# Kernel tuning notes

Measured on AMD Instinct MI355X. Metric: run time of the kernel, lower is better.

## Reference

```python
import jax, jax.numpy as jnp
import numpy as np

B, N, D, FF = 4096, 8, 256, 2048
EPS = 1e-5


def _layernorm(x, gamma, beta):
    mu = jnp.mean(x, axis=-1, keepdims=True)
    var = jnp.mean((x - mu) ** 2, axis=-1, keepdims=True)
    return (x - mu) * jax.lax.rsqrt(var + EPS) * gamma + beta


def _tt_product(x, w):
    # x: [b, d_in, n], w: [d_in, d_out, n]
    # h[:, :, k] = sum_i x[:, :, i] @ w[:, :, (k - i) % n]  (circular contraction)
    n = x.shape[-1]
    k = jnp.arange(n)
    idx = (k[:, None] - k[None, :]) % n          # [k, i]
    wg = w[:, :, idx]                            # [d_in, d_out, k, i]
    return jnp.einsum('bdi,doki->bok', x, wg)    # [b, d_out, n]


def setup_inputs() -> dict:
    key = jax.random.key(0)
    ks = jax.random.split(key, 12)
    xav = lambda k, shp, fi, fo: jax.random.uniform(k, shp, jnp.float32, -1.0, 1.0) * np.sqrt(6.0 / (fi + fo))
    return {
        'ent_seq': jax.random.normal(ks[0], (B, N, D), jnp.float32),
        'w_in': xav(ks[1], (D, D, N), D, D),
        'w_out': xav(ks[2], (D, D, N), D, D),
        'W1': xav(ks[3], (FF, D), D, FF),
        'bias1': jnp.zeros((FF,), jnp.float32),
        'W2': xav(ks[4], (D, FF), FF, D),
        'bias2': jnp.zeros((D,), jnp.float32),
        'gamma1': jnp.ones((D,), jnp.float32),
        'beta1': jnp.zeros((D,), jnp.float32),
        'gamma2': jnp.ones((D,), jnp.float32),
        'beta2': jnp.zeros((D,), jnp.float32),
    }


def reference(ent_seq, w_in, w_out, W1, bias1, W2, bias2, gamma1, beta1, gamma2, beta2):
    # self-attention-like block (dropout = identity in eval mode)
    xn = _layernorm(ent_seq, gamma1, beta1)          # [B, N, D]
    xp = jnp.transpose(xn, (0, 2, 1))                # [B, D, N]
    half = xp.shape[0] // 2
    h = jnp.concatenate([_tt_product(xp[:half], w_in),
                         _tt_product(xp[half:], w_out)], axis=0)
    x = ent_seq + jnp.transpose(h, (0, 2, 1))        # residual
    # FFN block
    yn = _layernorm(x, gamma2, beta2)
    ff = jax.nn.relu(yn @ W1.T + bias1) @ W2.T + bias2
    return x + ff
```

## Files before the change

### kernel.cpp

```cpp
#include <hip/hip_runtime.h>
#include <hip/hip_bf16.h>

typedef unsigned short ushort_t;
typedef __attribute__((ext_vector_type(8))) short bf16x8;
typedef __attribute__((ext_vector_type(4))) float f32x4;

#define B_SZ 4096
#define N_SZ 8
#define D_SZ 256
#define FF_SZ 2048
#define M_SZ (B_SZ * N_SZ)
#define WELEM (D_SZ * D_SZ * N_SZ)

__device__ inline float b2f(ushort_t u) {
    union { unsigned int i; float f; } t; t.i = ((unsigned int)u) << 16; return t.f;
}
__device__ inline ushort_t f2b(float f) {
    union { unsigned int i; float f; } t; t.f = f;
    unsigned int i = t.i;
    unsigned int r = (i + 0x7fffu + ((i >> 16) & 1u)) >> 16;
    return (ushort_t)r;
}

__device__ inline void gl2lds16(const ushort_t* g, ushort_t* l) {
    __builtin_amdgcn_global_load_lds((const __attribute__((address_space(1))) void*)g,
                                     (__attribute__((address_space(3))) void*)l, 16, 0, 0);
}

__global__ __launch_bounds__(256) void convert_weights(const float* __restrict__ w_in,
                                                       const float* __restrict__ w_out,
                                                       const float* __restrict__ W1,
                                                       const float* __restrict__ W2,
                                                       ushort_t* __restrict__ bt_in,
                                                       ushort_t* __restrict__ bt_out,
                                                       ushort_t* __restrict__ W1b,
                                                       ushort_t* __restrict__ W2b) {
    __shared__ float tile[64][65];
    const int bid = blockIdx.x;
    const int t = threadIdx.x;
    if (bid < 256) {
        const float* w = (bid < 128) ? w_in : w_out;
        ushort_t* bt = (bid < 128) ? bt_in : bt_out;
        const int id = bid & 127;
        const int d10 = (id >> 5) * 64;
        const int j0  = (id & 31) * 64;
#pragma unroll
        for (int it = 0; it < 16; ++it) {
            const int d1l = it * 4 + (t >> 6);
            const int jl = t & 63;
            tile[d1l][jl] = w[(size_t)(d10 + d1l) * 2048 + j0 + jl];
        }
        __syncthreads();
#pragma unroll
        for (int it = 0; it < 16; ++it) {
            const int jl = it * 4 + (t >> 6);
            const int d1l = t & 63;
            const int j = j0 + jl;
            bt[(size_t)(j >> 3) * 2048 + (j & 7) * 256 + d10 + d1l] = f2b(tile[d1l][jl]);
        }
    } else {
        const int id = bid - 256;
        const float* w = (id < 256) ? W1 : W2;
        ushort_t* o = (id < 256) ? W1b : W2b;
        const size_t base = (size_t)(id & 255) * 2048 + t * 8;
        const float4 a = *(const float4*)&w[base];
        const float4 b = *(const float4*)&w[base + 4];
        *(ushort4*)&o[base]     = make_ushort4(f2b(a.x), f2b(a.y), f2b(a.z), f2b(a.w));
        *(ushort4*)&o[base + 4] = make_ushort4(f2b(b.x), f2b(b.y), f2b(b.z), f2b(b.w));
    }
}

__global__ __launch_bounds__(256) void ln_fast(const float* __restrict__ xin,
                                               const float* __restrict__ gam,
                                               const float* __restrict__ bet,
                                               ushort_t* __restrict__ out) {
    const int wave = threadIdx.x >> 6;
    const int lane = threadIdx.x & 63;
    const size_t row = (size_t)blockIdx.x * 4 + wave;
    const float4 v = *(const float4*)&xin[row * 256 + lane * 4];
    float s = v.x + v.y + v.z + v.w;
    float q = v.x * v.x + v.y * v.y + v.z * v.z + v.w * v.w;
#pragma unroll
    for (int off = 1; off < 64; off <<= 1) {
        s += __shfl_xor(s, off, 64);
        q += __shfl_xor(q, off, 64);
    }
    const float mu = s * (1.0f / 256.0f);
    const float var = q * (1.0f / 256.0f) - mu * mu;
    const float rs = rsqrtf(var + 1e-5f);
    const float4 g = *(const float4*)&gam[lane * 4];
    const float4 b = *(const float4*)&bet[lane * 4];
    ushort4 o;
    o.x = f2b((v.x - mu) * rs * g.x + b.x);
    o.y = f2b((v.y - mu) * rs * g.y + b.y);
    o.z = f2b((v.z - mu) * rs * g.z + b.z);
    o.w = f2b((v.w - mu) * rs * g.w + b.w);
    *(ushort4*)&out[row * 256 + lane * 4] = o;
}

__global__ __launch_bounds__(256, 2) void tt_ln2(const ushort_t* __restrict__ A,
                                                 const ushort_t* __restrict__ Bt0,
                                                 const ushort_t* __restrict__ Bt1,
                                                 const float* __restrict__ g2,
                                                 const float* __restrict__ be2,
                                                 const float* __restrict__ entf,
                                                 ushort_t* __restrict__ yn,
                                                 ushort_t* __restrict__ xb) {
    __shared__ __attribute__((aligned(16))) ushort_t As[64 * 64];
    __shared__ __attribute__((aligned(16))) ushort_t Bs[256 * 64];
    __shared__ float red_s[64 * 4];
    __shared__ float red_q[64 * 4];

    const int t = threadIdx.x;
    const int lb = ((blockIdx.x & 1) << 8) | (blockIdx.x >> 1);
    const int m0 = lb * 64;
    const int lane = t & 63;
    const int wc = t >> 6;
    const int l16 = lane & 15, quad = lane >> 4;
    const int tr = t >> 3;
    const int csw = (((t & 7) ^ (tr & 7)) << 3);

    const ushort_t* Bt = (m0 >= M_SZ / 2) ? Bt1 : Bt0;

    f32x4 acc[4][4];
#pragma unroll
    for (int i = 0; i < 4; i++)
#pragma unroll
        for (int j = 0; j < 4; j++) acc[i][j] = (f32x4)(0.0f);

#pragma unroll 1
    for (int kt = 0; kt < 32; ++kt) {
        const int kg = kt * 64;
        __syncthreads();
#pragma unroll
        for (int p = 0; p < 2; ++p) {
            const int mrow = m0 + p * 32 + tr;
            const int kcol = kg + csw;
            const int s = kcol >> 8;
            const ushort_t* gA = A + (size_t)((mrow & ~7) + (((mrow & 7) - s) & 7)) * 256 + (kcol & 255);
            gl2lds16(gA, As + p * 2048 + t * 8);
        }
#pragma unroll
        for (int p = 0; p < 8; ++p) {
            gl2lds16(Bt + (size_t)(p * 32 + tr) * 2048 + kg + csw, Bs + p * 2048 + t * 8);
        }
        __syncthreads();

#pragma unroll
        for (int kk = 0; kk < 2; ++kk) {
            const int ac = ((((kk << 2) | quad) ^ (l16 & 7)) << 3);
            bf16x8 af[4], bfv[4];
#pragma unroll
            for (int i = 0; i < 4; i++) af[i]  = *(const bf16x8*)&As[(i * 16 + l16) * 64 + ac];
#pragma unroll
            for (int j = 0; j < 4; j++) bfv[j] = *(const bf16x8*)&Bs[(wc * 64 + j * 16 + l16) * 64 + ac];
#pragma unroll
            for (int i = 0; i < 4; i++)
#pragma unroll
                for (int j = 0; j < 4; j++)
                    acc[i][j] = __builtin_amdgcn_mfma_f32_16x16x32_bf16(af[i], bfv[j], acc[i][j], 0, 0, 0);
        }
    }

    int c[4];
#pragma unroll
    for (int j = 0; j < 4; j++) c[j] = wc * 64 + j * 16 + l16;
#pragma unroll
    for (int i = 0; i < 4; i++) {
#pragma unroll
        for (int r = 0; r < 4; r++) {
            const int rl = i * 16 + quad * 4 + r;
            const size_t grow = (size_t)(m0 + rl) * 256;
            float s = 0.0f, q = 0.0f;
#pragma unroll
            for (int j = 0; j < 4; j++) {
                float v = acc[i][j][r] + entf[grow + c[j]];
                acc[i][j][r] = v;
                s += v;
                q += v * v;
            }
#pragma unroll
            for (int off = 1; off < 16; off <<= 1) {
                s += __shfl_xor(s, off, 64);
                q += __shfl_xor(q, off, 64);
            }
            if (l16 == 0) { red_s[rl * 4 + wc] = s; red_q[rl * 4 + wc] = q; }
        }
    }
    __syncthreads();
#pragma unroll
    for (int i = 0; i < 4; i++) {
#pragma unroll
        for (int r = 0; r < 4; r++) {
            const int rl = i * 16 + quad * 4 + r;
            const size_t grow = (size_t)(m0 + rl) * 256;
            const float4 ss = *(const float4*)&red_s[rl * 4];
            const float4 qq = *(const float4*)&red_q[rl * 4];
            const float S = ss.x + ss.y + ss.z + ss.w;
            const float Q = qq.x + qq.y + qq.z + qq.w;
            const float mu = S * (1.0f / 256.0f);
            const float var = Q * (1.0f / 256.0f) - mu * mu;
            const float rs = rsqrtf(var + 1e-5f);
#pragma unroll
            for (int j = 0; j < 4; j++) {
                const float v = acc[i][j][r];
                yn[grow + c[j]] = f2b((v - mu) * rs * g2[c[j]] + be2[c[j]]);
                xb[grow + c[j]] = f2b(v);
            }
        }
    }
}

__global__ __launch_bounds__(256, 2) void ff_fused(const ushort_t* __restrict__ yn,
                                                   const ushort_t* __restrict__ W1b,
                                                   const ushort_t* __restrict__ W2b,
                                                   const float* __restrict__ bias1,
                                                   const float* __restrict__ bias2,
                                                   const ushort_t* __restrict__ xb,
                                                   float* __restrict__ out) {
    __shared__ __attribute__((aligned(16))) ushort_t As[64 * 64];
    __shared__ __attribute__((aligned(16))) ushort_t Bs[256 * 64];
    __shared__ __attribute__((aligned(16))) ushort_t Hc[64 * 256];

    const int t = threadIdx.x;
    const int m0 = blockIdx.x * 64;
    const int lane = t & 63;
    const int wc = t >> 6;
    const int l16 = lane & 15, quad = lane >> 4;
    const int tr = t >> 3;
    const int csw = (((t & 7) ^ (tr & 7)) << 3);

    f32x4 acc2[4][4];
#pragma unroll
    for (int i = 0; i < 4; i++)
#pragma unroll
        for (int j = 0; j < 4; j++) acc2[i][j] = (f32x4)(0.0f);

    int c4[4];
#pragma unroll
    for (int j = 0; j < 4; j++) c4[j] = wc * 64 + j * 16 + l16;

#pragma unroll 1
    for (int c = 0; c < 8; ++c) {
        f32x4 acc1[4][4];
#pragma unroll
        for (int i = 0; i < 4; i++)
#pragma unroll
            for (int j = 0; j < 4; j++) acc1[i][j] = (f32x4)(0.0f);

#pragma unroll 1
        for (int kb = 0; kb < 4; ++kb) {
            const int kg = kb * 64;
            __syncthreads();
#pragma unroll
            for (int p = 0; p < 2; ++p)
                gl2lds16(yn + (size_t)(m0 + p * 32 + tr) * 256 + kg + csw, As + p * 2048 + t * 8);
#pragma unroll
            for (int p = 0; p < 8; ++p)
                gl2lds16(W1b + (size_t)(c * 256 + p * 32 + tr) * 256 + kg + csw, Bs + p * 2048 + t * 8);
            __syncthreads();
#pragma unroll
            for (int kk = 0; kk < 2; ++kk) {
                const int ac = ((((kk << 2) | quad) ^ (l16 & 7)) << 3);
                bf16x8 af[4], bfv[4];
#pragma unroll
                for (int i = 0; i < 4; i++) af[i]  = *(const bf16x8*)&As[(i * 16 + l16) * 64 + ac];
#pragma unroll
                for (int j = 0; j < 4; j++) bfv[j] = *(const bf16x8*)&Bs[(wc * 64 + j * 16 + l16) * 64 + ac];
#pragma unroll
                for (int i = 0; i < 4; i++)
#pragma unroll
                    for (int j = 0; j < 4; j++)
                        acc1[i][j] = __builtin_amdgcn_mfma_f32_16x16x32_bf16(af[i], bfv[j], acc1[i][j], 0, 0, 0);
            }
        }

#pragma unroll
        for (int j = 0; j < 4; j++) {
            const float bb = bias1[c * 256 + c4[j]];
#pragma unroll
            for (int i = 0; i < 4; i++) {
                const int rbase = i * 16 + quad * 4;
#pragma unroll
                for (int r = 0; r < 4; r++) {
                    const int row = rbase + r;
                    float v = acc1[i][j][r] + bb;
                    v = v > 0.0f ? v : 0.0f;
                    Hc[row * 256 + (c4[j] ^ ((row & 7) << 3))] = f2b(v);
                }
            }
        }

#pragma unroll 1
        for (int kb = 0; kb < 4; ++kb) {
            __syncthreads();
#pragma unroll
            for (int p = 0; p < 8; ++p)
                gl2lds16(W2b + (size_t)(p * 32 + tr) * 2048 + c * 256 + kb * 64 + csw, Bs + p * 2048 + t * 8);
            __syncthreads();
#pragma unroll
            for (int kk = 0; kk < 2; ++kk) {
                const int ank = kb * 64 + (((kk << 2) | quad) << 3);
                const int ah  = ank ^ ((l16 & 7) << 3);
                const int ac  = ((((kk << 2) | quad) ^ (l16 & 7)) << 3);
                bf16x8 af[4], bfv[4];
#pragma unroll
                for (int i = 0; i < 4; i++) af[i]  = *(const bf16x8*)&Hc[(i * 16 + l16) * 256 + ah];
#pragma unroll
                for (int j = 0; j < 4; j++) bfv[j] = *(const bf16x8*)&Bs[(wc * 64 + j * 16 + l16) * 64 + ac];
#pragma unroll
                for (int i = 0; i < 4; i++)
#pragma unroll
                    for (int j = 0; j < 4; j++)
                        acc2[i][j] = __builtin_amdgcn_mfma_f32_16x16x32_bf16(af[i], bfv[j], acc2[i][j], 0, 0, 0);
            }
        }
    }

#pragma unroll
    for (int j = 0; j < 4; j++) {
        const float b2 = bias2[c4[j]];
#pragma unroll
        for (int i = 0; i < 4; i++) {
            const int rbase = m0 + i * 16 + quad * 4;
#pragma unroll
            for (int r = 0; r < 4; r++) {
                const size_t o = (size_t)(rbase + r) * 256 + c4[j];
                out[o] = acc2[i][j][r] + b2 + b2f(xb[o]);
            }
        }
    }
}

extern "C" void kernel_launch(void* const* d_in, const int* in_sizes, int n_in,
                              void* d_out, int out_size, void* d_ws, size_t ws_size,
                              hipStream_t stream) {
    const float* ent   = (const float*)d_in[0];
    const float* w_in  = (const float*)d_in[1];
    const float* w_out = (const float*)d_in[2];
    const float* W1    = (const float*)d_in[3];
    const float* bias1 = (const float*)d_in[4];
    const float* W2    = (const float*)d_in[5];
    const float* bias2 = (const float*)d_in[6];
    const float* g1    = (const float*)d_in[7];
    const float* be1   = (const float*)d_in[8];
    const float* g2    = (const float*)d_in[9];
    const float* be2   = (const float*)d_in[10];
    float* out = (float*)d_out;

    char* ws = (char*)d_ws;
    ushort_t* xn     = (ushort_t*)ws;
    ushort_t* yn     = (ushort_t*)(ws + 16777216);
    ushort_t* xb     = (ushort_t*)(ws + 2 * 16777216);
    ushort_t* bt_in  = (ushort_t*)(ws + 3 * 16777216);
    ushort_t* bt_out = bt_in + WELEM;
    ushort_t* W1b    = bt_out + WELEM;
    ushort_t* W2b    = W1b + WELEM;

    convert_weights<<<dim3(768), dim3(256), 0, stream>>>(w_in, w_out, W1, W2,
                                                         bt_in, bt_out, W1b, W2b);
    ln_fast<<<dim3(M_SZ / 4), dim3(256), 0, stream>>>(ent, g1, be1, xn);
    tt_ln2<<<dim3(M_SZ / 64), dim3(256), 0, stream>>>(xn, bt_in, bt_out, g2, be2, ent, yn, xb);
    ff_fused<<<dim3(M_SZ / 64), dim3(256), 0, stream>>>(yn, W1b, W2b, bias1, bias2, xb, out);
}
```

Measured before the change: 244.2 us.

## Split fused FFN into two large-tile GEMMs with an HBM hidden buffer

When the workspace is large enough, a new 256x256-tile, 512-thread kernel with double-buffered LDS staging replaces the circular-contraction kernel. The fused FFN is also split into two separate large-tile GEMM kernels that pass the ReLU hidden activations through a bf16 buffer in global memory. The aim is more data reuse per block and simpler GEMM loops. The cost is a large extra HBM round trip for the hidden tensor, much higher LDS use per block, and only 128 blocks for two of the kernels, which may leave many CUs idle.

```diff
diff --git a/kernel.cpp b/kernel.cpp
--- a/kernel.cpp
+++ b/kernel.cpp
@@ -98,6 +98,279 @@
     *(ushort4*)&out[row * 256 + lane * 4] = o;
 }
 
+
+__global__ __launch_bounds__(512, 2) void tt_ln2_v2(const ushort_t* __restrict__ A,
+                                                    const ushort_t* __restrict__ Bt0,
+                                                    const ushort_t* __restrict__ Bt1,
+                                                    const float* __restrict__ g2,
+                                                    const float* __restrict__ be2,
+                                                    const float* __restrict__ entf,
+                                                    ushort_t* __restrict__ yn,
+                                                    ushort_t* __restrict__ xb) {
+    __shared__ __attribute__((aligned(16))) ushort_t As[2][256 * 64];
+    __shared__ __attribute__((aligned(16))) ushort_t Bs[2][256 * 64];
+    __shared__ float red_s[256 * 4];
+    __shared__ float red_q[256 * 4];
+
+    const int t = threadIdx.x;
+    const int lb = ((blockIdx.x & 1) << 6) | (blockIdx.x >> 1);
+    const int m0 = lb * 256;
+    const int lane = t & 63;
+    const int wave = t >> 6;
+    const int wr = wave >> 2, wc = wave & 3;
+    const int l16 = lane & 15, quad = lane >> 4;
+    const int tr = t >> 3;
+    const int csw = (((t & 7) ^ (tr & 7)) << 3);
+
+    const ushort_t* Bt = (m0 >= M_SZ / 2) ? Bt1 : Bt0;
+
+    f32x4 acc[8][4];
+#pragma unroll
+    for (int i = 0; i < 8; i++)
+#pragma unroll
+        for (int j = 0; j < 4; j++) acc[i][j] = (f32x4)(0.0f);
+
+    auto stage = [&](int kt) {
+        ushort_t* a = As[kt & 1];
+        ushort_t* b = Bs[kt & 1];
+        const int kg = kt * 64;
+#pragma unroll
+        for (int p = 0; p < 4; ++p) {
+            const int mrow = m0 + p * 64 + tr;
+            const int kcol = kg + csw;
+            const int s = kcol >> 8;
+            const ushort_t* gA = A + (size_t)((mrow & ~7) + (((mrow & 7) - s) & 7)) * 256 + (kcol & 255);
+            gl2lds16(gA, a + p * 4096 + t * 8);
+        }
+#pragma unroll
+        for (int p = 0; p < 4; ++p) {
+            gl2lds16(Bt + (size_t)(p * 64 + tr) * 2048 + kg + csw, b + p * 4096 + t * 8);
+        }
+    };
+
+    stage(0);
+#pragma unroll 1
+    for (int kt = 0; kt < 32; ++kt) {
+        __syncthreads();
+        if (kt < 31) stage(kt + 1);
+        const ushort_t* a = As[kt & 1];
+        const ushort_t* b = Bs[kt & 1];
+#pragma unroll
+        for (int kk = 0; kk < 2; ++kk) {
+            const int ac = ((((kk << 2) | quad) ^ (l16 & 7)) << 3);
+            bf16x8 af[8], bfv[4];
+#pragma unroll
+            for (int i = 0; i < 8; i++) af[i]  = *(const bf16x8*)&a[(wr * 128 + i * 16 + l16) * 64 + ac];
+#pragma unroll
+            for (int j = 0; j < 4; j++) bfv[j] = *(const bf16x8*)&b[(wc * 64 + j * 16 + l16) * 64 + ac];
+#pragma unroll
+            for (int i = 0; i < 8; i++)
+#pragma unroll
+                for (int j = 0; j < 4; j++)
+                    acc[i][j] = __builtin_amdgcn_mfma_f32_16x16x32_bf16(af[i], bfv[j], acc[i][j], 0, 0, 0);
+        }
+    }
+
+    int c4[4];
+#pragma unroll
+    for (int j = 0; j < 4; j++) c4[j] = wc * 64 + j * 16 + l16;
+#pragma unroll
+    for (int i = 0; i < 8; i++) {
+#pragma unroll
+        for (int r = 0; r < 4; r++) {
+            const int rl = wr * 128 + i * 16 + quad * 4 + r;
+            const size_t grow = (size_t)(m0 + rl) * 256;
+            float s = 0.0f, q = 0.0f;
+#pragma unroll
+            for (int j = 0; j < 4; j++) {
+                float v = acc[i][j][r] + entf[grow + c4[j]];
+                acc[i][j][r] = v;
+                s += v;
+                q += v * v;
+            }
+#pragma unroll
+            for (int off = 1; off < 16; off <<= 1) {
+                s += __shfl_xor(s, off, 64);
+                q += __shfl_xor(q, off, 64);
+            }
+            if (l16 == 0) { red_s[rl * 4 + wc] = s; red_q[rl * 4 + wc] = q; }
+        }
+    }
+    __syncthreads();
+#pragma unroll
+    for (int i = 0; i < 8; i++) {
+#pragma unroll
+        for (int r = 0; r < 4; r++) {
+            const int rl = wr * 128 + i * 16 + quad * 4 + r;
+            const size_t grow = (size_t)(m0 + rl) * 256;
+            const float4 ss = *(const float4*)&red_s[rl * 4];
+            const float4 qq = *(const float4*)&red_q[rl * 4];
+            const float S = ss.x + ss.y + ss.z + ss.w;
+            const float Q = qq.x + qq.y + qq.z + qq.w;
+            const float mu = S * (1.0f / 256.0f);
+            const float var = Q * (1.0f / 256.0f) - mu * mu;
+            const float rs = rsqrtf(var + 1e-5f);
+#pragma unroll
+            for (int j = 0; j < 4; j++) {
+                const float v = acc[i][j][r];
+                yn[grow + c4[j]] = f2b((v - mu) * rs * g2[c4[j]] + be2[c4[j]]);
+                xb[grow + c4[j]] = f2b(v);
+            }
+        }
+    }
+}
+
+__global__ __launch_bounds__(512, 2) void ff_g1(const ushort_t* __restrict__ yn,
+                                                const ushort_t* __restrict__ W1b,
+                                                const float* __restrict__ bias1,
+                                                ushort_t* __restrict__ H) {
+    __shared__ __attribute__((aligned(16))) ushort_t As[2][256 * 64];
+    __shared__ __attribute__((aligned(16))) ushort_t Bs[2][256 * 64];
+
+    const int t = threadIdx.x;
+    const int ntile = blockIdx.x >> 7;
+    const int mtile = blockIdx.x & 127;
+    const int m0 = mtile * 256;
+    const int n0 = ntile * 256;
+    const int lane = t & 63;
+    const int wave = t >> 6;
+    const int wr = wave >> 2, wc = wave & 3;
+    const int l16 = lane & 15, quad = lane >> 4;
+    const int tr = t >> 3;
+    const int csw = (((t & 7) ^ (tr & 7)) << 3);
+
+    f32x4 acc[8][4];
+#pragma unroll
+    for (int i = 0; i < 8; i++)
+#pragma unroll
+        for (int j = 0; j < 4; j++) acc[i][j] = (f32x4)(0.0f);
+
+    auto stage = [&](int kt) {
+        ushort_t* a = As[kt & 1];
+        ushort_t* b = Bs[kt & 1];
+        const int kg = kt * 64;
+#pragma unroll
+        for (int p = 0; p < 4; ++p)
+            gl2lds16(yn + (size_t)(m0 + p * 64 + tr) * 256 + kg + csw, a + p * 4096 + t * 8);
+#pragma unroll
+        for (int p = 0; p < 4; ++p)
+            gl2lds16(W1b + (size_t)(n0 + p * 64 + tr) * 256 + kg + csw, b + p * 4096 + t * 8);
+    };
+
+    stage(0);
+#pragma unroll 1
+    for (int kt = 0; kt < 4; ++kt) {
+        __syncthreads();
+        if (kt < 3) stage(kt + 1);
+        const ushort_t* a = As[kt & 1];
+        const ushort_t* b = Bs[kt & 1];
+#pragma unroll
+        for (int kk = 0; kk < 2; ++kk) {
+            const int ac = ((((kk << 2) | quad) ^ (l16 & 7)) << 3);
+            bf16x8 af[8], bfv[4];
+#pragma unroll
+            for (int i = 0; i < 8; i++) af[i]  = *(const bf16x8*)&a[(wr * 128 + i * 16 + l16) * 64 + ac];
+#pragma unroll
+            for (int j = 0; j < 4; j++) bfv[j] = *(const bf16x8*)&b[(wc * 64 + j * 16 + l16) * 64 + ac];
+#pragma unroll
+            for (int i = 0; i < 8; i++)
+#pragma unroll
+                for (int j = 0; j < 4; j++)
+                    acc[i][j] = __builtin_amdgcn_mfma_f32_16x16x32_bf16(af[i], bfv[j], acc[i][j], 0, 0, 0);
+        }
+    }
+
+#pragma unroll
+    for (int j = 0; j < 4; j++) {
+        const int col = n0 + wc * 64 + j * 16 + l16;
+        const float bb = bias1[col];
+#pragma unroll
+        for (int i = 0; i < 8; i++) {
+            const int rbase = m0 + wr * 128 + i * 16 + quad * 4;
+#pragma unroll
+            for (int r = 0; r < 4; r++) {
+                float v = acc[i][j][r] + bb;
+                v = v > 0.0f ? v : 0.0f;
+                H[(size_t)(rbase + r) * 2048 + col] = f2b(v);
+            }
+        }
+    }
+}
+
+__global__ __launch_bounds__(512, 2) void ff_g2(const ushort_t* __restrict__ H,
+                                                const ushort_t* __restrict__ W2b,
+                                                const float* __restrict__ bias2,
+                                                const ushort_t* __restrict__ xb,
+                                                float* __restrict__ out) {
+    __shared__ __attribute__((aligned(16))) ushort_t As[2][256 * 64];
+    __shared__ __attribute__((aligned(16))) ushort_t Bs[2][256 * 64];
+
+    const int t = threadIdx.x;
+    const int m0 = blockIdx.x * 256;
+    const int lane = t & 63;
+    const int wave = t >> 6;
+    const int wr = wave >> 2, wc = wave & 3;
+    const int l16 = lane & 15, quad = lane >> 4;
+    const int tr = t >> 3;
+    const int csw = (((t & 7) ^ (tr & 7)) << 3);
+
+    f32x4 acc[8][4];
+#pragma unroll
+    for (int i = 0; i < 8; i++)
+#pragma unroll
+        for (int j = 0; j < 4; j++) acc[i][j] = (f32x4)(0.0f);
+
+    auto stage = [&](int kt) {
+        ushort_t* a = As[kt & 1];
+        ushort_t* b = Bs[kt & 1];
+        const int kg = kt * 64;
+#pragma unroll
+        for (int p = 0; p < 4; ++p)
+            gl2lds16(H + (size_t)(m0 + p * 64 + tr) * 2048 + kg + csw, a + p * 4096 + t * 8);
+#pragma unroll
+        for (int p = 0; p < 4; ++p)
+            gl2lds16(W2b + (size_t)(p * 64 + tr) * 2048 + kg + csw, b + p * 4096 + t * 8);
+    };
+
+    stage(0);
+#pragma unroll 1
+    for (int kt = 0; kt < 32; ++kt) {
+        __syncthreads();
+        if (kt < 31) stage(kt + 1);
+        const ushort_t* a = As[kt & 1];
+        const ushort_t* b = Bs[kt & 1];
+#pragma unroll
+        for (int kk = 0; kk < 2; ++kk) {
+            const int ac = ((((kk << 2) | quad) ^ (l16 & 7)) << 3);
+            bf16x8 af[8], bfv[4];
+#pragma unroll
+            for (int i = 0; i < 8; i++) af[i]  = *(const bf16x8*)&a[(wr * 128 + i * 16 + l16) * 64 + ac];
+#pragma unroll
+            for (int j = 0; j < 4; j++) bfv[j] = *(const bf16x8*)&b[(wc * 64 + j * 16 + l16) * 64 + ac];
+#pragma unroll
+            for (int i = 0; i < 8; i++)
+#pragma unroll
+                for (int j = 0; j < 4; j++)
+                    acc[i][j] = __builtin_amdgcn_mfma_f32_16x16x32_bf16(af[i], bfv[j], acc[i][j], 0, 0, 0);
+        }
+    }
+
+#pragma unroll
+    for (int j = 0; j < 4; j++) {
+        const int col = wc * 64 + j * 16 + l16;
+        const float b2 = bias2[col];
+#pragma unroll
+        for (int i = 0; i < 8; i++) {
+            const int rbase = m0 + wr * 128 + i * 16 + quad * 4;
+#pragma unroll
+            for (int r = 0; r < 4; r++) {
+                const size_t o = (size_t)(rbase + r) * 256 + col;
+                out[o] = acc[i][j][r] + b2 + b2f(xb[o]);
+            }
+        }
+    }
+}
+
 __global__ __launch_bounds__(256, 2) void tt_ln2(const ushort_t* __restrict__ A,
                                                  const ushort_t* __restrict__ Bt0,
                                                  const ushort_t* __restrict__ Bt1,
@@ -356,10 +629,21 @@
     ushort_t* bt_out = bt_in + WELEM;
     ushort_t* W1b    = bt_out + WELEM;
     ushort_t* W2b    = W1b + WELEM;
+    ushort_t* Hbuf   = (ushort_t*)(ws + 54525952);
+
+    const size_t need = 54525952ull + (size_t)M_SZ * FF_SZ * 2ull;
+    const bool big = (ws_size >= need);
 
     convert_weights<<<dim3(768), dim3(256), 0, stream>>>(w_in, w_out, W1, W2,
                                                          bt_in, bt_out, W1b, W2b);
     ln_fast<<<dim3(M_SZ / 4), dim3(256), 0, stream>>>(ent, g1, be1, xn);
-    tt_ln2<<<dim3(M_SZ / 64), dim3(256), 0, stream>>>(xn, bt_in, bt_out, g2, be2, ent, yn, xb);
-    ff_fused<<<dim3(M_SZ / 64), dim3(256), 0, stream>>>(yn, W1b, W2b, bias1, bias2, xb, out);
-}
+
+    if (big) {
+        tt_ln2_v2<<<dim3(M_SZ / 256), dim3(512), 0, stream>>>(xn, bt_in, bt_out, g2, be2, ent, yn, xb);
+        ff_g1<<<dim3((M_SZ / 256) * (FF_SZ / 256)), dim3(512), 0, stream>>>(yn, W1b, bias1, Hbuf);
+        ff_g2<<<dim3(M_SZ / 256), dim3(512), 0, stream>>>(Hbuf, W2b, bias2, xb, out);
+    } else {
+        tt_ln2<<<dim3(M_SZ / 64), dim3(256), 0, stream>>>(xn, bt_in, bt_out, g2, be2, ent, yn, xb);
+        ff_fused<<<dim3(M_SZ / 64), dim3(256), 0, stream>>>(yn, W1b, W2b, bias1, bias2, xb, out);
+    }
+}
```

New measurement: 340.7 us. 1.39x slower.

## Split TT GEMM along K and unfuse FFN into pipelined 256x256 GEMM kernels

Applied to the files above, without the earlier changes.

Replaces the 64-row fused kernels with 256x256-tile, 512-thread GEMM kernels. Each kernel uses a 4-stage global-to-LDS prefetch ring with explicit vmcnt waits and raised MFMA priority. The TT product is split into two K halves that write fp32 partials, and a separate combine kernel adds them with the residual and applies LayerNorm2. The FFN is split into a GEMM1+ReLU kernel that writes the full hidden activation H to global memory and a GEMM2 kernel that reads it back. The aim is better data reuse per tile and better latency hiding. The cost is extra global traffic for P and H, and the second FFN GEMM launches only 128 blocks.

```diff
diff --git a/kernel.cpp b/kernel.cpp
--- a/kernel.cpp
+++ b/kernel.cpp
@@ -26,6 +26,9 @@
     __builtin_amdgcn_global_load_lds((const __attribute__((address_space(1))) void*)g,
                                      (__attribute__((address_space(3))) void*)l, 16, 0, 0);
 }
+
+#define BAR()      __builtin_amdgcn_s_barrier()
+#define WAITV(n)   asm volatile("s_waitcnt vmcnt(" #n ")" ::: "memory")
 
 __global__ __launch_bounds__(256) void convert_weights(const float* __restrict__ w_in,
                                                        const float* __restrict__ w_out,
@@ -98,235 +101,272 @@
     *(ushort4*)&out[row * 256 + lane * 4] = o;
 }
 
-__global__ __launch_bounds__(256, 2) void tt_ln2(const ushort_t* __restrict__ A,
-                                                 const ushort_t* __restrict__ Bt0,
-                                                 const ushort_t* __restrict__ Bt1,
-                                                 const float* __restrict__ g2,
-                                                 const float* __restrict__ be2,
-                                                 const float* __restrict__ entf,
-                                                 ushort_t* __restrict__ yn,
-                                                 ushort_t* __restrict__ xb) {
-    __shared__ __attribute__((aligned(16))) ushort_t As[64 * 64];
-    __shared__ __attribute__((aligned(16))) ushort_t Bs[256 * 64];
-    __shared__ float red_s[64 * 4];
-    __shared__ float red_q[64 * 4];
+
+#define WAITV_SCHED(kt, NT) \
+    do { if ((kt) + 3 < (NT)) { stage((kt) + 3); WAITV(12); } \
+         else if ((kt) + 2 < (NT)) WAITV(8); \
+         else if ((kt) + 1 < (NT)) WAITV(4); \
+         else WAITV(0); } while (0)
+
+__global__ __launch_bounds__(512, 2) void tt_ks(const ushort_t* __restrict__ A,
+                                                const ushort_t* __restrict__ Bt0,
+                                                const ushort_t* __restrict__ Bt1,
+                                                float* __restrict__ P) {
+    __shared__ __attribute__((aligned(16))) ushort_t As[4][256 * 32];
+    __shared__ __attribute__((aligned(16))) ushort_t Bs[4][256 * 32];
 
     const int t = threadIdx.x;
-    const int lb = ((blockIdx.x & 1) << 8) | (blockIdx.x >> 1);
-    const int m0 = lb * 64;
-    const int lane = t & 63;
-    const int wc = t >> 6;
+    const int mtile = blockIdx.x & 127;
+    const int kh = blockIdx.x >> 7;
+    const int m0 = mtile * 256;
+    const int k0 = kh * 1024;
+    const int lane = t & 63, wave = t >> 6;
+    const int wr = wave >> 2, wc = wave & 3;
     const int l16 = lane & 15, quad = lane >> 4;
-    const int tr = t >> 3;
-    const int csw = (((t & 7) ^ (tr & 7)) << 3);
+    const int r  = t >> 2;
+    const int ssl = (t & 3) ^ (r & 3);
 
     const ushort_t* Bt = (m0 >= M_SZ / 2) ? Bt1 : Bt0;
-
-    f32x4 acc[4][4];
-#pragma unroll
-    for (int i = 0; i < 4; i++)
+    float* Pk = P + (size_t)kh * M_SZ * 256;
+
+    f32x4 acc[8][4];
+#pragma unroll
+    for (int i = 0; i < 8; i++)
 #pragma unroll
         for (int j = 0; j < 4; j++) acc[i][j] = (f32x4)(0.0f);
 
+    auto stage = [&](int kt) {
+        const int q = kt & 3;
+        const int kg = k0 + kt * 32;
+        const int s8 = kg >> 8;
+        const int kc = (kg & 255) + ssl * 8;
+#pragma unroll
+        for (int p = 0; p < 2; ++p) {
+            const int mrow = m0 + p * 128 + r;
+            const ushort_t* gA = A + (size_t)((mrow & ~7) + (((mrow & 7) - s8) & 7)) * 256 + kc;
+            gl2lds16(gA, &As[q][p * 4096 + t * 8]);
+        }
+#pragma unroll
+        for (int p = 0; p < 2; ++p) {
+            gl2lds16(Bt + (size_t)(p * 128 + r) * 2048 + kg + ssl * 8, &Bs[q][p * 4096 + t * 8]);
+        }
+    };
+
+    stage(0); stage(1); stage(2);
+    const int aoff = ((quad ^ (l16 & 3)) << 3);
 #pragma unroll 1
     for (int kt = 0; kt < 32; ++kt) {
-        const int kg = kt * 64;
-        __syncthreads();
-#pragma unroll
-        for (int p = 0; p < 2; ++p) {
-            const int mrow = m0 + p * 32 + tr;
-            const int kcol = kg + csw;
-            const int s = kcol >> 8;
-            const ushort_t* gA = A + (size_t)((mrow & ~7) + (((mrow & 7) - s) & 7)) * 256 + (kcol & 255);
-            gl2lds16(gA, As + p * 2048 + t * 8);
-        }
-#pragma unroll
-        for (int p = 0; p < 8; ++p) {
-            gl2lds16(Bt + (size_t)(p * 32 + tr) * 2048 + kg + csw, Bs + p * 2048 + t * 8);
-        }
-        __syncthreads();
-
-#pragma unroll
-        for (int kk = 0; kk < 2; ++kk) {
-            const int ac = ((((kk << 2) | quad) ^ (l16 & 7)) << 3);
-            bf16x8 af[4], bfv[4];
-#pragma unroll
-            for (int i = 0; i < 4; i++) af[i]  = *(const bf16x8*)&As[(i * 16 + l16) * 64 + ac];
-#pragma unroll
-            for (int j = 0; j < 4; j++) bfv[j] = *(const bf16x8*)&Bs[(wc * 64 + j * 16 + l16) * 64 + ac];
-#pragma unroll
-            for (int i = 0; i < 4; i++)
-#pragma unroll
-                for (int j = 0; j < 4; j++)
-                    acc[i][j] = __builtin_amdgcn_mfma_f32_16x16x32_bf16(af[i], bfv[j], acc[i][j], 0, 0, 0);
-        }
-    }
-
-    int c[4];
-#pragma unroll
-    for (int j = 0; j < 4; j++) c[j] = wc * 64 + j * 16 + l16;
-#pragma unroll
-    for (int i = 0; i < 4; i++) {
-#pragma unroll
-        for (int r = 0; r < 4; r++) {
-            const int rl = i * 16 + quad * 4 + r;
-            const size_t grow = (size_t)(m0 + rl) * 256;
-            float s = 0.0f, q = 0.0f;
-#pragma unroll
-            for (int j = 0; j < 4; j++) {
-                float v = acc[i][j][r] + entf[grow + c[j]];
-                acc[i][j][r] = v;
-                s += v;
-                q += v * v;
+        BAR();
+        WAITV_SCHED(kt, 32);
+        BAR();
+        const ushort_t* a = As[kt & 3];
+        const ushort_t* b = Bs[kt & 3];
+        bf16x8 af[8], bfv[4];
+#pragma unroll
+        for (int i = 0; i < 8; i++) af[i]  = *(const bf16x8*)&a[(wr * 128 + i * 16 + l16) * 32 + aoff];
+#pragma unroll
+        for (int j = 0; j < 4; j++) bfv[j] = *(const bf16x8*)&b[(wc * 64 + j * 16 + l16) * 32 + aoff];
+        __builtin_amdgcn_s_setprio(1);
+#pragma unroll
+        for (int i = 0; i < 8; i++)
+#pragma unroll
+            for (int j = 0; j < 4; j++)
+                acc[i][j] = __builtin_amdgcn_mfma_f32_16x16x32_bf16(af[i], bfv[j], acc[i][j], 0, 0, 0);
+        __builtin_amdgcn_s_setprio(0);
+    }
+
+#pragma unroll
+    for (int j = 0; j < 4; j++) {
+        const int coln = wc * 64 + j * 16 + l16;
+#pragma unroll
+        for (int i = 0; i < 8; i++) {
+            const int rbase = m0 + wr * 128 + i * 16 + quad * 4;
+#pragma unroll
+            for (int rr = 0; rr < 4; rr++)
+                Pk[(size_t)(rbase + rr) * 256 + coln] = acc[i][j][rr];
+        }
+    }
+}
+
+__global__ __launch_bounds__(256) void tt_combine(const float* __restrict__ P,
+                                                  const float* __restrict__ ent,
+                                                  const float* __restrict__ g2,
+                                                  const float* __restrict__ be2,
+                                                  ushort_t* __restrict__ yn,
+                                                  ushort_t* __restrict__ xb) {
+    const int wave = threadIdx.x >> 6;
+    const int lane = threadIdx.x & 63;
+    const size_t row = (size_t)blockIdx.x * 4 + wave;
+    const size_t o = row * 256 + lane * 4;
+    const float4 a = *(const float4*)&P[o];
+    const float4 b = *(const float4*)&P[(size_t)M_SZ * 256 + o];
+    const float4 e = *(const float4*)&ent[o];
+    float4 v;
+    v.x = a.x + b.x + e.x; v.y = a.y + b.y + e.y;
+    v.z = a.z + b.z + e.z; v.w = a.w + b.w + e.w;
+    float s = v.x + v.y + v.z + v.w;
+    float q = v.x * v.x + v.y * v.y + v.z * v.z + v.w * v.w;
+#pragma unroll
+    for (int off = 1; off < 64; off <<= 1) {
+        s += __shfl_xor(s, off, 64);
+        q += __shfl_xor(q, off, 64);
+    }
+    const float mu = s * (1.0f / 256.0f);
+    const float var = q * (1.0f / 256.0f) - mu * mu;
+    const float rs = rsqrtf(var + 1e-5f);
+    const float4 g = *(const float4*)&g2[lane * 4];
+    const float4 be = *(const float4*)&be2[lane * 4];
+    ushort4 yo, xo;
+    yo.x = f2b((v.x - mu) * rs * g.x + be.x); xo.x = f2b(v.x);
+    yo.y = f2b((v.y - mu) * rs * g.y + be.y); xo.y = f2b(v.y);
+    yo.z = f2b((v.z - mu) * rs * g.z + be.z); xo.z = f2b(v.z);
+    yo.w = f2b((v.w - mu) * rs * g.w + be.w); xo.w = f2b(v.w);
+    *(ushort4*)&yn[o] = yo;
+    *(ushort4*)&xb[o] = xo;
+}
+
+__global__ __launch_bounds__(512, 2) void ff_g1(const ushort_t* __restrict__ yn,
+                                                const ushort_t* __restrict__ W1b,
+                                                const float* __restrict__ bias1,
+                                                ushort_t* __restrict__ H) {
+    __shared__ __attribute__((aligned(16))) ushort_t As[4][256 * 32];
+    __shared__ __attribute__((aligned(16))) ushort_t Bs[4][256 * 32];
+
+    const int t = threadIdx.x;
+    const int ntile = blockIdx.x >> 7;
+    const int mtile = blockIdx.x & 127;
+    const int m0 = mtile * 256;
+    const int n0 = ntile * 256;
+    const int lane = t & 63, wave = t >> 6;
+    const int wr = wave >> 2, wc = wave & 3;
+    const int l16 = lane & 15, quad = lane >> 4;
+    const int r  = t >> 2;
+    const int ssl = (t & 3) ^ (r & 3);
+
+    f32x4 acc[8][4];
+#pragma unroll
+    for (int i = 0; i < 8; i++)
+#pragma unroll
+        for (int j = 0; j < 4; j++) acc[i][j] = (f32x4)(0.0f);
+
+    auto stage = [&](int kt) {
+        const int q = kt & 3;
+        const int kg = kt * 32 + ssl * 8;
+#pragma unroll
+        for (int p = 0; p < 2; ++p)
+            gl2lds16(yn + (size_t)(m0 + p * 128 + r) * 256 + kg, &As[q][p * 4096 + t * 8]);
+#pragma unroll
+        for (int p = 0; p < 2; ++p)
+            gl2lds16(W1b + (size_t)(n0 + p * 128 + r) * 256 + kg, &Bs[q][p * 4096 + t * 8]);
+    };
+
+    stage(0); stage(1); stage(2);
+    const int aoff = ((quad ^ (l16 & 3)) << 3);
+#pragma unroll 1
+    for (int kt = 0; kt < 8; ++kt) {
+        BAR();
+        WAITV_SCHED(kt, 8);
+        BAR();
+        const ushort_t* a = As[kt & 3];
+        const ushort_t* b = Bs[kt & 3];
+        bf16x8 af[8], bfv[4];
+#pragma unroll
+        for (int i = 0; i < 8; i++) af[i]  = *(const bf16x8*)&a[(wr * 128 + i * 16 + l16) * 32 + aoff];
+#pragma unroll
+        for (int j = 0; j < 4; j++) bfv[j] = *(const bf16x8*)&b[(wc * 64 + j * 16 + l16) * 32 + aoff];
+        __builtin_amdgcn_s_setprio(1);
+#pragma unroll
+        for (int i = 0; i < 8; i++)
+#pragma unroll
+            for (int j = 0; j < 4; j++)
+                acc[i][j] = __builtin_amdgcn_mfma_f32_16x16x32_bf16(af[i], bfv[j], acc[i][j], 0, 0, 0);
+        __builtin_amdgcn_s_setprio(0);
+    }
+
+#pragma unroll
+    for (int j = 0; j < 4; j++) {
+        const int col = n0 + wc * 64 + j * 16 + l16;
+        const float bb = bias1[col];
+#pragma unroll
+        for (int i = 0; i < 8; i++) {
+            const int rbase = m0 + wr * 128 + i * 16 + quad * 4;
+#pragma unroll
+            for (int rr = 0; rr < 4; rr++) {
+                float v = acc[i][j][rr] + bb;
+                v = v > 0.0f ? v : 0.0f;
+                H[(size_t)(rbase + rr) * 2048 + col] = f2b(v);
             }
-#pragma unroll
-            for (int off = 1; off < 16; off <<= 1) {
-                s += __shfl_xor(s, off, 64);
-                q += __shfl_xor(q, off, 64);
-            }
-            if (l16 == 0) { red_s[rl * 4 + wc] = s; red_q[rl * 4 + wc] = q; }
-        }
-    }
-    __syncthreads();
-#pragma unroll
-    for (int i = 0; i < 4; i++) {
-#pragma unroll
-        for (int r = 0; r < 4; r++) {
-            const int rl = i * 16 + quad * 4 + r;
-            const size_t grow = (size_t)(m0 + rl) * 256;
-            const float4 ss = *(const float4*)&red_s[rl * 4];
-            const float4 qq = *(const float4*)&red_q[rl * 4];
-            const float S = ss.x + ss.y + ss.z + ss.w;
-            const float Q = qq.x + qq.y + qq.z + qq.w;
-            const float mu = S * (1.0f / 256.0f);
-            const float var = Q * (1.0f / 256.0f) - mu * mu;
-            const float rs = rsqrtf(var + 1e-5f);
-#pragma unroll
-            for (int j = 0; j < 4; j++) {
-                const float v = acc[i][j][r];
-                yn[grow + c[j]] = f2b((v - mu) * rs * g2[c[j]] + be2[c[j]]);
-                xb[grow + c[j]] = f2b(v);
-            }
-        }
-    }
-}
-
-__global__ __launch_bounds__(256, 2) void ff_fused(const ushort_t* __restrict__ yn,
-                                                   const ushort_t* __restrict__ W1b,
-                                                   const ushort_t* __restrict__ W2b,
-                                                   const float* __restrict__ bias1,
-                                                   const float* __restrict__ bias2,
-                                                   const ushort_t* __restrict__ xb,
-                                                   float* __restrict__ out) {
-    __shared__ __attribute__((aligned(16))) ushort_t As[64 * 64];
-    __shared__ __attribute__((aligned(16))) ushort_t Bs[256 * 64];
-    __shared__ __attribute__((aligned(16))) ushort_t Hc[64 * 256];
+        }
+    }
+}
+
+__global__ __launch_bounds__(512, 2) void ff_g2(const ushort_t* __restrict__ H,
+                                                const ushort_t* __restrict__ W2b,
+                                                const float* __restrict__ bias2,
+                                                const ushort_t* __restrict__ xb,
+                                                float* __restrict__ out) {
+    __shared__ __attribute__((aligned(16))) ushort_t As[4][256 * 32];
+    __shared__ __attribute__((aligned(16))) ushort_t Bs[4][256 * 32];
 
     const int t = threadIdx.x;
-    const int m0 = blockIdx.x * 64;
-    const int lane = t & 63;
-    const int wc = t >> 6;
+    const int m0 = blockIdx.x * 256;
+    const int lane = t & 63, wave = t >> 6;
+    const int wr = wave >> 2, wc = wave & 3;
     const int l16 = lane & 15, quad = lane >> 4;
-    const int tr = t >> 3;
-    const int csw = (((t & 7) ^ (tr & 7)) << 3);
-
-    f32x4 acc2[4][4];
-#pragma unroll
-    for (int i = 0; i < 4; i++)
-#pragma unroll
-        for (int j = 0; j < 4; j++) acc2[i][j] = (f32x4)(0.0f);
-
-    int c4[4];
-#pragma unroll
-    for (int j = 0; j < 4; j++) c4[j] = wc * 64 + j * 16 + l16;
-
+    const int r  = t >> 2;
+    const int ssl = (t & 3) ^ (r & 3);
+
+    f32x4 acc[8][4];
+#pragma unroll
+    for (int i = 0; i < 8; i++)
+#pragma unroll
+        for (int j = 0; j < 4; j++) acc[i][j] = (f32x4)(0.0f);
+
+    auto stage = [&](int kt) {
+        const int q = kt & 3;
+        const int kg = kt * 32 + ssl * 8;
+#pragma unroll
+        for (int p = 0; p < 2; ++p)
+            gl2lds16(H + (size_t)(m0 + p * 128 + r) * 2048 + kg, &As[q][p * 4096 + t * 8]);
+#pragma unroll
+        for (int p = 0; p < 2; ++p)
+            gl2lds16(W2b + (size_t)(p * 128 + r) * 2048 + kg, &Bs[q][p * 4096 + t * 8]);
+    };
+
+    stage(0); stage(1); stage(2);
+    const int aoff = ((quad ^ (l16 & 3)) << 3);
 #pragma unroll 1
-    for (int c = 0; c < 8; ++c) {
-        f32x4 acc1[4][4];
-#pragma unroll
-        for (int i = 0; i < 4; i++)
-#pragma unroll
-            for (int j = 0; j < 4; j++) acc1[i][j] = (f32x4)(0.0f);
-
-#pragma unroll 1
-        for (int kb = 0; kb < 4; ++kb) {
-            const int kg = kb * 64;
-            __syncthreads();
-#pragma unroll
-            for (int p = 0; p < 2; ++p)
-                gl2lds16(yn + (size_t)(m0 + p * 32 + tr) * 256 + kg + csw, As + p * 2048 + t * 8);
-#pragma unroll
-            for (int p = 0; p < 8; ++p)
-                gl2lds16(W1b + (size_t)(c * 256 + p * 32 + tr) * 256 + kg + csw, Bs + p * 2048 + t * 8);
-            __syncthreads();
-#pragma unroll
-            for (int kk = 0; kk < 2; ++kk) {
-                const int ac = ((((kk << 2) | quad) ^ (l16 & 7)) << 3);
-                bf16x8 af[4], bfv[4];
-#pragma unroll
-                for (int i = 0; i < 4; i++) af[i]  = *(const bf16x8*)&As[(i * 16 + l16) * 64 + ac];
-#pragma unroll
-                for (int j = 0; j < 4; j++) bfv[j] = *(const bf16x8*)&Bs[(wc * 64 + j * 16 + l16) * 64 + ac];
-#pragma unroll
-                for (int i = 0; i < 4; i++)
-#pragma unroll
-                    for (int j = 0; j < 4; j++)
-                        acc1[i][j] = __builtin_amdgcn_mfma_f32_16x16x32_bf16(af[i], bfv[j], acc1[i][j], 0, 0, 0);
-            }
-        }
-
-#pragma unroll
-        for (int j = 0; j < 4; j++) {
-            const float bb = bias1[c * 256 + c4[j]];
-#pragma unroll
-            for (int i = 0; i < 4; i++) {
-                const int rbase = i * 16 + quad * 4;
-#pragma unroll
-                for (int r = 0; r < 4; r++) {
-                    const int row = rbase + r;
-                    float v = acc1[i][j][r] + bb;
-                    v = v > 0.0f ? v : 0.0f;
-                    Hc[row * 256 + (c4[j] ^ ((row & 7) << 3))] = f2b(v);
-                }
-            }
-        }
-
-#pragma unroll 1
-        for (int kb = 0; kb < 4; ++kb) {
-            __syncthreads();
-#pragma unroll
-            for (int p = 0; p < 8; ++p)
-                gl2lds16(W2b + (size_t)(p * 32 + tr) * 2048 + c * 256 + kb * 64 + csw, Bs + p * 2048 + t * 8);
-            __syncthreads();
-#pragma unroll
-            for (int kk = 0; kk < 2; ++kk) {
-                const int ank = kb * 64 + (((kk << 2) | quad) << 3);
-                const int ah  = ank ^ ((l16 & 7) << 3);
-                const int ac  = ((((kk << 2) | quad) ^ (l16 & 7)) << 3);
-                bf16x8 af[4], bfv[4];
-#pragma unroll
-                for (int i = 0; i < 4; i++) af[i]  = *(const bf16x8*)&Hc[(i * 16 + l16) * 256 + ah];
-#pragma unroll
-                for (int j = 0; j < 4; j++) bfv[j] = *(const bf16x8*)&Bs[(wc * 64 + j * 16 + l16) * 64 + ac];
-#pragma unroll
-                for (int i = 0; i < 4; i++)
-#pragma unroll
-                    for (int j = 0; j < 4; j++)
-                        acc2[i][j] = __builtin_amdgcn_mfma_f32_16x16x32_bf16(af[i], bfv[j], acc2[i][j], 0, 0, 0);
-            }
-        }
+    for (int kt = 0; kt < 64; ++kt) {
+        BAR();
+        WAITV_SCHED(kt, 64);
+        BAR();
+        const ushort_t* a = As[kt & 3];
+        const ushort_t* b = Bs[kt & 3];
+        bf16x8 af[8], bfv[4];
+#pragma unroll
+        for (int i = 0; i < 8; i++) af[i]  = *(const bf16x8*)&a[(wr * 128 + i * 16 + l16) * 32 + aoff];
+#pragma unroll
+        for (int j = 0; j < 4; j++) bfv[j] = *(const bf16x8*)&b[(wc * 64 + j * 16 + l16) * 32 + aoff];
+        __builtin_amdgcn_s_setprio(1);
+#pragma unroll
+        for (int i = 0; i < 8; i++)
+#pragma unroll
+            for (int j = 0; j < 4; j++)
+                acc[i][j] = __builtin_amdgcn_mfma_f32_16x16x32_bf16(af[i], bfv[j], acc[i][j], 0, 0, 0);
+        __builtin_amdgcn_s_setprio(0);
     }
 
 #pragma unroll
     for (int j = 0; j < 4; j++) {
-        const float b2 = bias2[c4[j]];
-#pragma unroll
-        for (int i = 0; i < 4; i++) {
-            const int rbase = m0 + i * 16 + quad * 4;
-#pragma unroll
-            for (int r = 0; r < 4; r++) {
-                const size_t o = (size_t)(rbase + r) * 256 + c4[j];
-                out[o] = acc2[i][j][r] + b2 + b2f(xb[o]);
+        const int col = wc * 64 + j * 16 + l16;
+        const float b2 = bias2[col];
+#pragma unroll
+        for (int i = 0; i < 8; i++) {
+            const int rbase = m0 + wr * 128 + i * 16 + quad * 4;
+#pragma unroll
+            for (int rr = 0; rr < 4; rr++) {
+                const size_t o = (size_t)(rbase + rr) * 256 + col;
+                out[o] = acc[i][j][rr] + b2 + b2f(xb[o]);
             }
         }
     }
@@ -356,10 +396,14 @@
     ushort_t* bt_out = bt_in + WELEM;
     ushort_t* W1b    = bt_out + WELEM;
     ushort_t* W2b    = W1b + WELEM;
+    float*    P      = (float*)(ws + 54525952);
+    ushort_t* Hbuf   = (ushort_t*)(ws + 54525952);
 
     convert_weights<<<dim3(768), dim3(256), 0, stream>>>(w_in, w_out, W1, W2,
                                                          bt_in, bt_out, W1b, W2b);
     ln_fast<<<dim3(M_SZ / 4), dim3(256), 0, stream>>>(ent, g1, be1, xn);
-    tt_ln2<<<dim3(M_SZ / 64), dim3(256), 0, stream>>>(xn, bt_in, bt_out, g2, be2, ent, yn, xb);
-    ff_fused<<<dim3(M_SZ / 64), dim3(256), 0, stream>>>(yn, W1b, W2b, bias1, bias2, xb, out);
-}
+    tt_ks<<<dim3(256), dim3(512), 0, stream>>>(xn, bt_in, bt_out, P);
+    tt_combine<<<dim3(M_SZ / 4), dim3(256), 0, stream>>>(P, ent, g2, be2, yn, xb);
+    ff_g1<<<dim3(1024), dim3(512), 0, stream>>>(yn, W1b, bias1, Hbuf);
+    ff_g2<<<dim3(128), dim3(512), 0, stream>>>(Hbuf, W2b, bias2, xb, out);
+}
```

Measured after the change: 354.3 us. 45.1% more time.
